# Kernel optimization log

Measured on AMD Instinct MI355X. Metric: run time of the kernel, lower is better.

The kernel has to match this reference:

```python
import jax, jax.numpy as jnp
import numpy as np

B = 1048576
L = 32

def setup_inputs() -> dict:
    key = jax.random.key(0)
    k1, k2 = jax.random.split(key)
    D_pred_logit = jax.random.normal(k1, (B, L), dtype=jnp.float32)
    # D is a true distribution over L bins: random positives normalized per row
    raw = jax.random.uniform(k2, (B, L), dtype=jnp.float32)
    D = raw / jnp.sum(raw, axis=1, keepdims=True)
    return {"D_pred_logit": D_pred_logit, "D": D}

def reference(D_pred_logit, D):
    Lc = D.shape[1]
    # Ordinal similarity matrix A[j,k] = 1 - |j-k|/(L-1)  (PSD by construction)
    idx = jnp.arange(Lc, dtype=jnp.float32)
    A = 1.0 - jnp.abs(idx[:, None] - idx[None, :]) / (Lc - 1)
    A = A.astype(D.dtype)
    Q = D - jax.nn.softmax(D_pred_logit, axis=1)  # [B, L]
    # mean(diag(Q @ A @ Q^T)) == mean over rows of sum((Q @ A) * Q, axis=1)
    # (same math; avoids the B x B intermediate of the original)
    per_row = jnp.sum((Q @ A) * Q, axis=1)  # [B]
    return jnp.mean(per_row)
```

## Files before the change

kernel.cpp:

```cpp
#include <hip/hip_runtime.h>


#define L_BINS 32

__global__ void qfd2_init(double* acc) {
    if (threadIdx.x == 0 && blockIdx.x == 0) *acc = 0.0;
}

__global__ __launch_bounds__(256) void qfd2_main(const float* __restrict__ logit,
                                                 const float* __restrict__ D,
                                                 double* __restrict__ acc,
                                                 int n_groups) {
    const int tid     = blockIdx.x * blockDim.x + threadIdx.x;
    const int lane    = threadIdx.x & 63;
    const int wave    = tid >> 6;
    const int n_waves = (gridDim.x * blockDim.x) >> 6;
    const int c       = lane & 7;

    float acc_v = 0.0f;
    const float k31 = 2.0f / 31.0f;

    for (int g = wave; g < n_groups; g += n_waves) {
        const size_t base = (size_t)g * 256 + (size_t)lane * 4;
        const float4 z = *(const float4*)(logit + base);
        const float4 d = *(const float4*)(D + base);

        float m = fmaxf(fmaxf(z.x, z.y), fmaxf(z.z, z.w));
        m = fmaxf(m, __shfl_xor(m, 1));
        m = fmaxf(m, __shfl_xor(m, 2));
        m = fmaxf(m, __shfl_xor(m, 4));

        float e0 = __expf(z.x - m), e1 = __expf(z.y - m);
        float e2 = __expf(z.z - m), e3 = __expf(z.w - m);
        float s = e0 + e1 + e2 + e3;
        s += __shfl_xor(s, 1);
        s += __shfl_xor(s, 2);
        s += __shfl_xor(s, 4);
        const float rs = 1.0f / s;

        const float q0 = d.x - e0 * rs;
        const float q1 = d.y - e1 * rs;
        const float q2 = d.z - e2 * rs;
        const float q3 = d.w - e3 * rs;
        const float l0 = q0, l1 = q0 + q1, l2 = l1 + q2, l3 = l2 + q3;

        float inc = l3, t;
        t = __shfl_up(inc, 1, 8); if (c >= 1) inc += t;
        t = __shfl_up(inc, 2, 8); if (c >= 2) inc += t;
        t = __shfl_up(inc, 4, 8); if (c >= 4) inc += t;
        const float off = inc - l3;
        const float P0 = off + l0, P1 = off + l1, P2 = off + l2, P3 = inc;
        const float S = __shfl(inc, 7, 8);

        const bool last = (c == 7);
        const float sumP  = P0 + P1 + P2 + (last ? 0.0f : P3);
        const float sumP2 = P0 * P0 + P1 * P1 + P2 * P2 + (last ? 0.0f : P3 * P3);

        acc_v += k31 * (sumP2 - S * sumP) + 0.125f * S * S;
    }

    for (int msk = 1; msk < 64; msk <<= 1) acc_v += __shfl_xor(acc_v, msk);

    __shared__ float wpart[4];
    const int wib = threadIdx.x >> 6;
    if (lane == 0) wpart[wib] = acc_v;
    __syncthreads();
    if (threadIdx.x == 0) {
        const float bsum = wpart[0] + wpart[1] + wpart[2] + wpart[3];
        atomicAdd(acc, (double)bsum);
    }
}

__global__ void qfd2_finalize(const double* acc, float* out, int rows) {
    if (threadIdx.x == 0 && blockIdx.x == 0)
        out[0] = (float)(*acc / (double)rows);
}

extern "C" void kernel_launch(void* const* d_in, const int* in_sizes, int n_in,
                              void* d_out, int out_size, void* d_ws, size_t ws_size,
                              hipStream_t stream) {
    const float* logit = (const float*)d_in[0];
    const float* D     = (const float*)d_in[1];
    float* out         = (float*)d_out;
    double* acc        = (double*)d_ws;

    const int rows     = in_sizes[0] / L_BINS;
    const int n_groups = rows / 8;

    qfd2_init<<<1, 64, 0, stream>>>(acc);
    qfd2_main<<<4096, 256, 0, stream>>>(logit, D, acc, n_groups);
    qfd2_finalize<<<1, 64, 0, stream>>>(acc, out, rows);
}
```

Measured before the change: 281.4 us.

## Map one row per thread and replace atomics with two-pass partial reduction

Each thread now owns a full 32-bin row and does max, exp, sum and the prefix-sum quadratic form serially in registers, so the cross-lane shuffles used before for per-row reductions and scans are gone. The grid becomes one block per 256 rows instead of a grid-stride loop. Per-block partials are written to the workspace and summed in double by a single finalize block, which drops the init kernel and the atomic. The cost is that each thread loads eight strided float4s per input, which coalesces less well than the old layout, and register pressure rises.

Result: no change. 276.9 us (-1.6%).

```diff
diff --git a/kernel.cpp b/kernel.cpp
--- a/kernel.cpp
+++ b/kernel.cpp
@@ -1,79 +1,89 @@
 #include <hip/hip_runtime.h>
 
 
-#define L_BINS 32
+#define L_BINS  32
+#define NTHREAD 256
 
-__global__ void qfd2_init(double* acc) {
-    if (threadIdx.x == 0 && blockIdx.x == 0) *acc = 0.0;
+__global__ __launch_bounds__(NTHREAD) void qfd2_main(const float* __restrict__ logit,
+                                                     const float* __restrict__ D,
+                                                     float* __restrict__ partial,
+                                                     int rows) {
+    const int row = blockIdx.x * NTHREAD + threadIdx.x;
+    float res = 0.0f;
+
+    if (row < rows) {
+        const float4* zp = (const float4*)(logit + (size_t)row * L_BINS);
+        const float4* dp = (const float4*)(D     + (size_t)row * L_BINS);
+
+        float z[L_BINS], d[L_BINS];
+        float4* zv = (float4*)z;
+        float4* dv = (float4*)d;
+#pragma unroll
+        for (int i = 0; i < 8; ++i) zv[i] = zp[i];
+#pragma unroll
+        for (int i = 0; i < 8; ++i) dv[i] = dp[i];
+
+        float t[16];
+#pragma unroll
+        for (int i = 0; i < 16; ++i) t[i] = fmaxf(z[i], z[i + 16]);
+#pragma unroll
+        for (int i = 0; i < 8; ++i)  t[i] = fmaxf(t[i], t[i + 8]);
+#pragma unroll
+        for (int i = 0; i < 4; ++i)  t[i] = fmaxf(t[i], t[i + 4]);
+        t[0] = fmaxf(t[0], t[2]);
+        t[1] = fmaxf(t[1], t[3]);
+        const float m = fmaxf(t[0], t[1]);
+
+        float e[L_BINS];
+#pragma unroll
+        for (int i = 0; i < L_BINS; ++i) e[i] = __expf(z[i] - m);
+
+        float u[16];
+#pragma unroll
+        for (int i = 0; i < 16; ++i) u[i] = e[i] + e[i + 16];
+#pragma unroll
+        for (int i = 0; i < 8; ++i)  u[i] = u[i] + u[i + 8];
+#pragma unroll
+        for (int i = 0; i < 4; ++i)  u[i] = u[i] + u[i + 4];
+        const float s  = (u[0] + u[2]) + (u[1] + u[3]);
+        const float rs = 1.0f / s;
+
+        float P = 0.0f, sP = 0.0f, sP2 = 0.0f;
+#pragma unroll
+        for (int i = 0; i < L_BINS - 1; ++i) {
+            P  += d[i] - e[i] * rs;
+            sP += P;
+            sP2 = fmaf(P, P, sP2);
+        }
+        P += d[L_BINS - 1] - e[L_BINS - 1] * rs;
+        const float S = P;
+        res = (2.0f / 31.0f) * (sP2 - S * sP) + S * S;
+    }
+
+#pragma unroll
+    for (int msk = 1; msk < 64; msk <<= 1) res += __shfl_xor(res, msk);
+
+    __shared__ float wpart[NTHREAD / 64];
+    const int wib = threadIdx.x >> 6;
+    if ((threadIdx.x & 63) == 0) wpart[wib] = res;
+    __syncthreads();
+    if (threadIdx.x == 0)
+        partial[blockIdx.x] = (wpart[0] + wpart[1]) + (wpart[2] + wpart[3]);
 }
 
-__global__ __launch_bounds__(256) void qfd2_main(const float* __restrict__ logit,
-                                                 const float* __restrict__ D,
-                                                 double* __restrict__ acc,
-                                                 int n_groups) {
-    const int tid     = blockIdx.x * blockDim.x + threadIdx.x;
-    const int lane    = threadIdx.x & 63;
-    const int wave    = tid >> 6;
-    const int n_waves = (gridDim.x * blockDim.x) >> 6;
-    const int c       = lane & 7;
+__global__ __launch_bounds__(256) void qfd2_fin(const float* __restrict__ partial,
+                                                float* __restrict__ out,
+                                                int nblocks, int rows) {
+    double a = 0.0;
+    for (int i = threadIdx.x; i < nblocks; i += 256) a += (double)partial[i];
+#pragma unroll
+    for (int msk = 1; msk < 64; msk <<= 1) a += __shfl_xor(a, msk);
 
-    float acc_v = 0.0f;
-    const float k31 = 2.0f / 31.0f;
-
-    for (int g = wave; g < n_groups; g += n_waves) {
-        const size_t base = (size_t)g * 256 + (size_t)lane * 4;
-        const float4 z = *(const float4*)(logit + base);
-        const float4 d = *(const float4*)(D + base);
-
-        float m = fmaxf(fmaxf(z.x, z.y), fmaxf(z.z, z.w));
-        m = fmaxf(m, __shfl_xor(m, 1));
-        m = fmaxf(m, __shfl_xor(m, 2));
-        m = fmaxf(m, __shfl_xor(m, 4));
-
-        float e0 = __expf(z.x - m), e1 = __expf(z.y - m);
-        float e2 = __expf(z.z - m), e3 = __expf(z.w - m);
-        float s = e0 + e1 + e2 + e3;
-        s += __shfl_xor(s, 1);
-        s += __shfl_xor(s, 2);
-        s += __shfl_xor(s, 4);
-        const float rs = 1.0f / s;
-
-        const float q0 = d.x - e0 * rs;
-        const float q1 = d.y - e1 * rs;
-        const float q2 = d.z - e2 * rs;
-        const float q3 = d.w - e3 * rs;
-        const float l0 = q0, l1 = q0 + q1, l2 = l1 + q2, l3 = l2 + q3;
-
-        float inc = l3, t;
-        t = __shfl_up(inc, 1, 8); if (c >= 1) inc += t;
-        t = __shfl_up(inc, 2, 8); if (c >= 2) inc += t;
-        t = __shfl_up(inc, 4, 8); if (c >= 4) inc += t;
-        const float off = inc - l3;
-        const float P0 = off + l0, P1 = off + l1, P2 = off + l2, P3 = inc;
-        const float S = __shfl(inc, 7, 8);
-
-        const bool last = (c == 7);
-        const float sumP  = P0 + P1 + P2 + (last ? 0.0f : P3);
-        const float sumP2 = P0 * P0 + P1 * P1 + P2 * P2 + (last ? 0.0f : P3 * P3);
-
-        acc_v += k31 * (sumP2 - S * sumP) + 0.125f * S * S;
-    }
-
-    for (int msk = 1; msk < 64; msk <<= 1) acc_v += __shfl_xor(acc_v, msk);
-
-    __shared__ float wpart[4];
-    const int wib = threadIdx.x >> 6;
-    if (lane == 0) wpart[wib] = acc_v;
+    __shared__ double wp[4];
+    if ((threadIdx.x & 63) == 0) wp[threadIdx.x >> 6] = a;
     __syncthreads();
-    if (threadIdx.x == 0) {
-        const float bsum = wpart[0] + wpart[1] + wpart[2] + wpart[3];
-        atomicAdd(acc, (double)bsum);
-    }
-}
-
-__global__ void qfd2_finalize(const double* acc, float* out, int rows) {
-    if (threadIdx.x == 0 && blockIdx.x == 0)
-        out[0] = (float)(*acc / (double)rows);
+    if (threadIdx.x == 0)
+        out[0] = (float)(((wp[0] + wp[1]) + (wp[2] + wp[3])) / (double)rows);
 }
 
 extern "C" void kernel_launch(void* const* d_in, const int* in_sizes, int n_in,
@@ -82,12 +92,11 @@
     const float* logit = (const float*)d_in[0];
     const float* D     = (const float*)d_in[1];
     float* out         = (float*)d_out;
-    double* acc        = (double*)d_ws;
+    float* partial     = (float*)d_ws;
 
-    const int rows     = in_sizes[0] / L_BINS;
-    const int n_groups = rows / 8;
+    const int rows    = in_sizes[0] / L_BINS;
+    const int nblocks = (rows + NTHREAD - 1) / NTHREAD;
 
-    qfd2_init<<<1, 64, 0, stream>>>(acc);
-    qfd2_main<<<4096, 256, 0, stream>>>(logit, D, acc, n_groups);
-    qfd2_finalize<<<1, 64, 0, stream>>>(acc, out, rows);
+    qfd2_main<<<nblocks, NTHREAD, 0, stream>>>(logit, D, partial, rows);
+    qfd2_fin<<<1, 256, 0, stream>>>(partial, out, nblocks, rows);
 }
```
